# Kernel tuning notes

Hardware: AMD Instinct MI355X
Metric: run time of the kernel (lower is better)

The kernel has to match this reference:

```python
import jax, jax.numpy as jnp
import numpy as np

B, U1, U2 = 2, 3072, 3072
IF = 256      # in_feat_dim
FD = 256      # feat_dim
M = 4         # num_modes
D = IF // M   # attention_mode_dim = 64
STD = 0.02    # base_initializer_range
LN_EPS = 1e-12


def setup_inputs() -> dict:
    key = jax.random.key(0)
    ks = jax.random.split(key, 8)
    inp = {
        'query_feat': jax.random.normal(ks[0], (B, U1, IF), jnp.float32),
        'key_feat':   jax.random.normal(ks[1], (B, U2, IF), jnp.float32),
        # tied QK projection (key weight == query weight after tie_qk)
        'Wq':    jax.random.normal(ks[2], (M * D, IF), jnp.float32) * STD,
        # value projection of ExpandedFeatTrans.first_linear (v_has_bias=True)
        'Wv':    jax.random.normal(ks[3], (M * FD, IF), jnp.float32) * STD,
        'bv':    jnp.zeros((M * FD,), jnp.float32),
        # MMSharedMid shared linear
        'W_mid': jax.random.normal(ks[4], (FD, FD), jnp.float32) * STD,
        'b_mid': jnp.zeros((FD,), jnp.float32),
        # MMSharedOutput shared linear + LayerNorm
        'W_out': jax.random.normal(ks[5], (FD, FD), jnp.float32) * STD,
        'b_out': jnp.zeros((FD,), jnp.float32),
        'ln_g':  jnp.ones((FD,), jnp.float32),
        'ln_b':  jnp.zeros((FD,), jnp.float32),
        # LearnedSoftAggregate feat2score linear (FD -> 1)
        'W_agg': jax.random.normal(ks[6], (1, FD), jnp.float32) * STD,
        'b_agg': jnp.zeros((1,), jnp.float32),
    }
    return inp


def _layer_norm(x, g, b):
    mu = x.mean(-1, keepdims=True)
    var = ((x - mu) ** 2).mean(-1, keepdims=True)
    return (x - mu) * jax.lax.rsqrt(var + LN_EPS) * g + b


def reference(query_feat, key_feat, Wq, Wv, bv, W_mid, b_mid, W_out, b_out,
              ln_g, ln_b, W_agg, b_agg):
    # --- multi-mode cross attention with tied QK ---
    q = (query_feat @ Wq.T).reshape(B, U1, M, D).transpose(0, 2, 1, 3)  # b m u d
    k = (key_feat   @ Wq.T).reshape(B, U2, M, D).transpose(0, 2, 1, 3)  # b m v d
    scores = jnp.einsum('bmud,bmvd->bmuv', q, k) / np.float32(np.sqrt(D))
    probs = jax.nn.softmax(scores, axis=-1)                              # b m u v

    # --- ExpandedFeatTrans: per-mode value projection + fusion ---
    v = (key_feat @ Wv.T + bv).reshape(B, U2, M, FD).transpose(0, 2, 1, 3)  # b m v f
    fused = jnp.einsum('bmuv,bmvf->bmuf', probs, v)                          # b m u f

    # --- MMSharedMid FFN (shared linear + exact gelu; dropout=0) ---
    mid = jax.nn.gelu(fused @ W_mid.T + b_mid, approximate=False)

    # --- MMSharedOutput: shared linear + residual + LayerNorm ---
    outp = _layer_norm(mid @ W_out.T + b_out + fused, ln_g, ln_b)            # b m u f

    # --- LearnedSoftAggregate over modes (group_dim=1) ---
    mode_scores = (outp @ W_agg.T + b_agg)[..., 0]                           # b m u
    agg_probs = jax.nn.softmax(mode_scores, axis=1)
    trans_feat = (outp * agg_probs[..., None]).sum(axis=1)                   # b u f
    return trans_feat
```

## Files before the change

kernel.cpp:

```cpp
#include <hip/hip_runtime.h>
#include <hip/hip_bf16.h>
#include <cstdint>
#include <cstddef>

typedef __attribute__((ext_vector_type(8))) short     bf16x8;
typedef __attribute__((ext_vector_type(4))) float     f32x4;
typedef __attribute__((ext_vector_type(4))) unsigned short u16x4;

using as1_void = __attribute__((address_space(1))) void;
using as3_void = __attribute__((address_space(3))) void;

#define MFMA16(a,b,c) __builtin_amdgcn_mfma_f32_16x16x32_bf16((a),(b),(c),0,0,0)

__device__ __forceinline__ unsigned short f2bf(float f) {
  union { float f; unsigned u; } v; v.f = f;
  unsigned r = v.u + 0x7fffu + ((v.u >> 16) & 1u);
  return (unsigned short)(r >> 16);
}
__device__ __forceinline__ float bf2f(unsigned short h) {
  union { unsigned u; float f; } v; v.u = ((unsigned)h) << 16; return v.f;
}
__device__ __forceinline__ unsigned cvt_pk_bf16(float lo, float hi) {
  unsigned r;
  asm volatile("v_cvt_pk_bf16_f32 %0, %1, %2" : "=v"(r) : "v"(lo), "v"(hi));
  return r;
}
__device__ __forceinline__ float fast_erf(float x) {
  float ax = fabsf(x);
  float t = __builtin_amdgcn_rcpf(fmaf(0.3275911f, ax, 1.0f));
  float p = fmaf(1.061405429f, t, -1.453152027f);
  p = fmaf(p, t, 1.421413741f);
  p = fmaf(p, t, -0.284496736f);
  p = fmaf(p, t, 0.254829592f);
  p = p * t;
  float e = __builtin_amdgcn_exp2f(-ax * ax * 1.44269504f);
  float r = fmaf(-p, e, 1.0f);
  return copysignf(r, x);
}

__device__ __forceinline__ void gload16(const void* g, void* l) {
  __builtin_amdgcn_global_load_lds((const as1_void*)g, (as3_void*)l, 16, 0, 0);
}

constexpr size_t oXq  = 0;
constexpr size_t oXk  = oXq + 1572864ull * 2;
constexpr size_t oWq  = oXk + 1572864ull * 2;
constexpr size_t oWv  = oWq + 65536ull   * 2;
constexpr size_t oWm  = oWv + 262144ull  * 2;
constexpr size_t oWo  = oWm + 65536ull   * 2;
constexpr size_t oQb  = oWo + 65536ull   * 2;
constexpr size_t oKb  = oQb + 1572864ull * 2;
constexpr size_t oVb  = oKb + 1572864ull * 2;
constexpr size_t oPa  = oVb + 6291456ull * 2;
constexpr size_t oMl  = oPa + 12582912ull * 2;

__global__ __launch_bounds__(256) void cvtw_kernel(
    const float* __restrict__ wq, const float* __restrict__ wv,
    const float* __restrict__ wm, const float* __restrict__ wo,
    char* __restrict__ wsb) {
  int i4 = (blockIdx.x * 256 + threadIdx.x) * 4;
  const float* src; size_t dsto; int local;
  if (i4 < 65536)        { src = wq; dsto = oWq; local = i4; }
  else if (i4 < 327680)  { src = wv; dsto = oWv; local = i4 - 65536; }
  else if (i4 < 393216)  { src = wm; dsto = oWm; local = i4 - 327680; }
  else                   { src = wo; dsto = oWo; local = i4 - 393216; }
  f32x4 v = *(const f32x4*)(src + local);
  u16x4 o;
  o.x = f2bf(v.x); o.y = f2bf(v.y); o.z = f2bf(v.z); o.w = f2bf(v.w);
  *(u16x4*)((unsigned short*)(wsb + dsto) + local) = o;
}

__global__ __launch_bounds__(256, 3) void proj_kernel(
    const float* __restrict__ qf32, const float* __restrict__ kf32,
    const float* __restrict__ bv, char* __restrict__ wsb) {
  __shared__ unsigned short sA[48 * 256];

  const int lane = threadIdx.x & 63, wid = threadIdx.x >> 6;
  const int lq = lane & 15, hi = lane >> 4;
  const int ny = blockIdx.x % 6;
  const int r0 = (blockIdx.x / 6) * 48;

  const float* Xf = (ny == 0) ? qf32 : kf32;
  const unsigned short* W;
  if (ny <= 1) W = (const unsigned short*)(wsb + oWq);
  else         W = (const unsigned short*)(wsb + oWv) + (size_t)(ny - 2) * 256 * 256;

  {
    const int t = threadIdx.x;
#pragma unroll
    for (int j = 0; j < 12; ++j) {
      int flat = j * 256 + t;
      int row = flat >> 6;
      int c4 = flat & 63;
      f32x4 v = *(const f32x4*)(Xf + ((size_t)(r0 + row) * 256 + c4 * 4));
      u16x4 o;
      o.x = f2bf(v.x); o.y = f2bf(v.y); o.z = f2bf(v.z); o.w = f2bf(v.w);
      int col = c4 * 4;
      int c8 = col >> 3;
      *(u16x4*)&sA[row * 256 + (((c8 ^ (row & 7)) << 3) + (col & 7))] = o;
    }
  }
  __syncthreads();

  const int n0 = wid * 64;

  f32x4 acc[3][4];
#pragma unroll
  for (int rg = 0; rg < 3; ++rg)
#pragma unroll
    for (int bt = 0; bt < 4; ++bt) acc[rg][bt] = (f32x4){0.f, 0.f, 0.f, 0.f};

#pragma unroll
  for (int ks = 0; ks < 8; ++ks) {
    bf16x8 a[3];
#pragma unroll
    for (int rg = 0; rg < 3; ++rg)
      a[rg] = *(const bf16x8*)&sA[(rg * 16 + lq) * 256 + (((ks * 4 + hi) ^ (lq & 7)) << 3)];
#pragma unroll
    for (int bt = 0; bt < 4; ++bt) {
      int n = n0 + bt * 16 + lq;
      bf16x8 bfr = *(const bf16x8*)(W + (size_t)n * 256 + ks * 32 + hi * 8);
#pragma unroll
      for (int rg = 0; rg < 3; ++rg) acc[rg][bt] = MFMA16(a[rg], bfr, acc[rg][bt]);
    }
  }

  const int b = r0 / 3072, u0 = r0 % 3072;

  if (ny <= 1) {
    unsigned short* outp = (unsigned short*)(wsb + (ny == 0 ? oQb : oKb));
    float scale = (ny == 0) ? 0.125f : 1.0f;
    int m = wid;
#pragma unroll
    for (int bt = 0; bt < 4; ++bt) {
      int d = bt * 16 + lq;
#pragma unroll
      for (int rg = 0; rg < 3; ++rg) {
        int ub = u0 + rg * 16 + hi * 4;
#pragma unroll
        for (int r = 0; r < 4; ++r) {
          outp[((size_t)(b * 4 + m) * 3072 + (ub + r)) * 64 + d] = f2bf(acc[rg][bt][r] * scale);
        }
      }
    }
  } else {
    unsigned short* vbT = (unsigned short*)(wsb + oVb);
    int mchunk = ny - 2;
#pragma unroll
    for (int bt = 0; bt < 4; ++bt) {
      int f = n0 + bt * 16 + lq;
      float bias = bv[mchunk * 256 + f];
#pragma unroll
      for (int rg = 0; rg < 3; ++rg) {
        int ub = u0 + rg * 16 + hi * 4;
        u16x4 pk;
#pragma unroll
        for (int r = 0; r < 4; ++r) pk[r] = f2bf(acc[rg][bt][r] + bias);
        *(u16x4*)(vbT + ((size_t)(b * 4 + mchunk) * 256 + f) * 3072 + ub) = pk;
      }
    }
  }
}

__global__ __launch_bounds__(256, 3) void attn_kernel(char* __restrict__ wsb) {
  __shared__ unsigned short sK[64 * 64];
  __shared__ unsigned short sV[256 * 64];
  __shared__ unsigned short sP[4][16 * 64];
  __shared__ float sCr[4];
  __shared__ float sInv[4][16];

  const int lane = threadIdx.x & 63, wid = threadIdx.x >> 6;
  const int lq = lane & 15, hi = lane >> 4;
  const int lr3 = lane >> 3, lc3 = lane & 7;
  const int fh = wid >> 1, gp = wid & 1;
  const int bm = blockIdx.x & 7;
  const int z = blockIdx.x >> 3;
  const int qt = z >> 1, kvh = z & 1;
  const int q0 = qt * 64;
  const int kvbase = kvh * 1536;
  const int key = lq & 7;

  const unsigned short* qb = (const unsigned short*)(wsb + oQb) + (size_t)bm * 3072 * 64;
  const unsigned short* kb = (const unsigned short*)(wsb + oKb) + (size_t)bm * 3072 * 64;
  const unsigned short* vb = (const unsigned short*)(wsb + oVb) + (size_t)bm * 256 * 3072;

  const unsigned short* qp = qb + (size_t)(q0 + wid * 16 + lq) * 64 + hi * 8;
  const bf16x8 qf0 = *(const bf16x8*)(qp);
  const bf16x8 qf1 = *(const bf16x8*)(qp + 32);

  const unsigned short* pk[2];
  unsigned short* dk[2];
#pragma unroll
  for (int i = 0; i < 2; ++i) {
    int ch = wid * 2 + i;
    int r = ch * 8 + lr3;
    int cs = lc3 ^ (r & 7);
    pk[i] = kb + (size_t)(kvbase + r) * 64 + cs * 8;
    dk[i] = &sK[ch * 512];
  }
  const unsigned short* pv[8];
  unsigned short* dv[8];
#pragma unroll
  for (int i = 0; i < 8; ++i) {
    int ch = i * 4 + wid;
    int f = ch * 8 + lr3;
    int cs = lc3 ^ (f & 7);
    pv[i] = vb + (size_t)f * 3072 + kvbase + cs * 8;
    dv[i] = &sV[ch * 512];
  }

  const int o0 = (hi ^ key) << 4;
  const int o1 = ((hi + 4) ^ key) << 4;
  const char* kB0 = (const char*)sK + lq * 128 + o0;
  const char* kB1 = (const char*)sK + lq * 128 + o1;
  const char* vB0 = (const char*)sV + (size_t)(fh * 128 + lq) * 128 + o0;
  const char* vB1 = (const char*)sV + (size_t)(fh * 128 + lq) * 128 + o1;
  char* myP = (char*)&sP[wid][0] + lq * 128;
  int wofs[4];
#pragma unroll
  for (int t = 0; t < 4; ++t)
    wofs[t] = ((((2 * t + (hi >> 1)) ^ key) << 4) + ((hi & 1) << 3));
  const int g0 = gp * 2, g1 = gp * 2 + 1;
  const char* rP0 = (const char*)&sP[g0][0] + lq * 128;
  const char* rP1 = (const char*)&sP[g1][0] + lq * 128;

  f32x4 acc[2][8];
#pragma unroll
  for (int g = 0; g < 2; ++g)
#pragma unroll
    for (int ft = 0; ft < 8; ++ft) acc[g][ft] = (f32x4){0.f, 0.f, 0.f, 0.f};
  float mrun = -1e30f, lrun = 0.f;

  gload16(pk[0], dk[0]); gload16(pk[1], dk[1]);
  pk[0] += 4096; pk[1] += 4096;
  asm volatile("s_waitcnt vmcnt(0)" ::: "memory");
  __builtin_amdgcn_sched_barrier(0);
  __builtin_amdgcn_s_barrier();

  for (int kt = 0; kt < 24; ++kt) {
#pragma unroll
    for (int i = 0; i < 8; ++i) { gload16(pv[i], dv[i]); pv[i] += 64; }

    bf16x8 kc0[4], kc1[4];
#pragma unroll
    for (int t = 0; t < 4; ++t) {
      kc0[t] = *(const bf16x8*)(kB0 + t * 2048);
      kc1[t] = *(const bf16x8*)(kB1 + t * 2048);
    }
    f32x4 s[4];
#pragma unroll
    for (int t = 0; t < 4; ++t) {
      f32x4 zz = (f32x4){0.f, 0.f, 0.f, 0.f};
      zz = MFMA16(kc0[t], qf0, zz);
      zz = MFMA16(kc1[t], qf1, zz);
      s[t] = zz;
    }

    float p0 = fmaxf(fmaxf(s[0][0], s[0][1]), fmaxf(s[0][2], s[0][3]));
    float p1 = fmaxf(fmaxf(s[1][0], s[1][1]), fmaxf(s[1][2], s[1][3]));
    float p2 = fmaxf(fmaxf(s[2][0], s[2][1]), fmaxf(s[2][2], s[2][3]));
    float p3 = fmaxf(fmaxf(s[3][0], s[3][1]), fmaxf(s[3][2], s[3][3]));
    float pmax = fmaxf(fmaxf(p0, p1), fmaxf(p2, p3));
    pmax = fmaxf(pmax, __shfl_xor(pmax, 16));
    pmax = fmaxf(pmax, __shfl_xor(pmax, 32));

    float cr = 1.0f;
    if (__any(pmax > mrun + 8.0f)) {
      float mnew = fmaxf(mrun, pmax);
      cr = __builtin_amdgcn_exp2f((mrun - mnew) * 1.44269504f);
      lrun *= cr; mrun = mnew;
    }
    if (lane == 0) sCr[wid] = cr;

    const float mk = mrun * 1.44269504f;
    float ps[4][4];
    float psum = 0.f;
#pragma unroll
    for (int t = 0; t < 4; ++t)
#pragma unroll
      for (int r = 0; r < 4; ++r) {
        float p = __builtin_amdgcn_exp2f(s[t][r] * 1.44269504f - mk);
        ps[t][r] = p; psum += p;
      }
    psum += __shfl_xor(psum, 16);
    psum += __shfl_xor(psum, 32);
    lrun += psum;

#pragma unroll
    for (int t = 0; t < 4; ++t) {
      unsigned w0 = cvt_pk_bf16(ps[t][0], ps[t][1]);
      unsigned w1 = cvt_pk_bf16(ps[t][2], ps[t][3]);
      *(uint2*)(myP + wofs[t]) = make_uint2(w0, w1);
    }

    asm volatile("s_waitcnt vmcnt(0) lgkmcnt(0)" ::: "memory");
    __builtin_amdgcn_sched_barrier(0);
    __builtin_amdgcn_s_barrier();

    if (kt < 23) {
      gload16(pk[0], dk[0]); gload16(pk[1], dk[1]);
      pk[0] += 4096; pk[1] += 4096;
    }

    float c0 = sCr[g0], c1 = sCr[g1];
    if (c0 != 1.0f) {
#pragma unroll
      for (int ft = 0; ft < 8; ++ft) {
        acc[0][ft][0] *= c0; acc[0][ft][1] *= c0;
        acc[0][ft][2] *= c0; acc[0][ft][3] *= c0;
      }
    }
    if (c1 != 1.0f) {
#pragma unroll
      for (int ft = 0; ft < 8; ++ft) {
        acc[1][ft][0] *= c1; acc[1][ft][1] *= c1;
        acc[1][ft][2] *= c1; acc[1][ft][3] *= c1;
      }
    }

    bf16x8 pb00 = *(const bf16x8*)(rP0 + o0);
    bf16x8 pb01 = *(const bf16x8*)(rP0 + o1);
    bf16x8 pb10 = *(const bf16x8*)(rP1 + o0);
    bf16x8 pb11 = *(const bf16x8*)(rP1 + o1);

    __builtin_amdgcn_s_setprio(1);
#pragma unroll
    for (int ft = 0; ft < 8; ++ft) {
      bf16x8 vf0 = *(const bf16x8*)(vB0 + ft * 2048);
      bf16x8 vf1 = *(const bf16x8*)(vB1 + ft * 2048);
      acc[0][ft] = MFMA16(vf0, pb00, acc[0][ft]);
      acc[0][ft] = MFMA16(vf1, pb01, acc[0][ft]);
      acc[1][ft] = MFMA16(vf0, pb10, acc[1][ft]);
      acc[1][ft] = MFMA16(vf1, pb11, acc[1][ft]);
    }
    __builtin_amdgcn_s_setprio(0);

    asm volatile("s_waitcnt vmcnt(0) lgkmcnt(0)" ::: "memory");
    __builtin_amdgcn_sched_barrier(0);
    __builtin_amdgcn_s_barrier();
  }

  if (hi == 0) {
    sInv[wid][lq] = 1.0f / lrun;
    float* ml = (float*)(wsb + oMl);
    size_t qi = (size_t)(kvh * 8 + bm) * 3072 + q0 + wid * 16 + lq;
    *(float2*)(ml + qi * 2) = make_float2(mrun, lrun);
  }
  __syncthreads();

  unsigned short* paB = (unsigned short*)(wsb + oPa) + (size_t)(kvh * 8 + bm) * 3072 * 256;
#pragma unroll
  for (int gi = 0; gi < 2; ++gi) {
    int g = gp * 2 + gi;
    float inv = sInv[g][lq];
    unsigned short* orow = paB + (size_t)(q0 + g * 16 + lq) * 256 + fh * 128 + hi * 4;
#pragma unroll
    for (int ft = 0; ft < 8; ++ft) {
      u16x4 pk4;
#pragma unroll
      for (int r = 0; r < 4; ++r) pk4[r] = f2bf(acc[gi][ft][r] * inv);
      *(u16x4*)(orow + ft * 16) = pk4;
    }
  }
}

__global__ __launch_bounds__(256, 3) void ffn_kernel(char* __restrict__ wsb,
                                                     const float* __restrict__ bmid,
                                                     const float* __restrict__ bout,
                                                     const float* __restrict__ lng,
                                                     const float* __restrict__ lnb,
                                                     const float* __restrict__ wagg,
                                                     const float* __restrict__ bagg,
                                                     float* __restrict__ out) {
  __shared__ unsigned short sA[32 * 256];
  __shared__ unsigned short sM[32 * 256];
  __shared__ float redS[4][32], redQ[4][32], redC[4][32];
  __shared__ float sSc[32];
  __shared__ float sW0[32], sW1[32];

  const int lane = threadIdx.x & 63, wid = threadIdx.x >> 6;
  const int lq = lane & 15, hi = lane >> 4;
  const int b = blockIdx.x / 384;
  const int u0 = (blockIdx.x % 384) * 8;

  const unsigned short* Wm = (const unsigned short*)(wsb + oWm);
  const unsigned short* Wo = (const unsigned short*)(wsb + oWo);
  const unsigned short* pa = (const unsigned short*)(wsb + oPa);
  const float* mlb = (const float*)(wsb + oMl);

  if (threadIdx.x < 32) {
    int m = threadIdx.x & 3, du = threadIdx.x >> 2;
    size_t qi = (size_t)(b * 4 + m) * 3072 + u0 + du;
    float2 ml0 = *(const float2*)(mlb + qi * 2);
    float2 ml1 = *(const float2*)(mlb + (qi + 8ull * 3072) * 2);
    float M = fmaxf(ml0.x, ml1.x);
    float e0 = ml0.y * __builtin_amdgcn_exp2f((ml0.x - M) * 1.44269504f);
    float e1 = ml1.y * __builtin_amdgcn_exp2f((ml1.x - M) * 1.44269504f);
    float inv = 1.0f / (e0 + e1);
    sW0[threadIdx.x] = e0 * inv;
    sW1[threadIdx.x] = e1 * inv;
  }
  __syncthreads();

  {
    int t = threadIdx.x;
#pragma unroll
    for (int j = 0; j < 4; ++j) {
      int i = j * 256 + t;
      int row = i >> 5, c = i & 31;
      int m = row & 3, du = row >> 2;
      const unsigned short* p0 = pa + ((size_t)(b * 4 + m) * 3072 + u0 + du) * 256 + c * 8;
      bf16x8 a = *(const bf16x8*)(p0);
      bf16x8 bb = *(const bf16x8*)(p0 + 8ull * 3072 * 256);
      float w0 = sW0[row], w1 = sW1[row];
      u16x4 oA, oB;
#pragma unroll
      for (int e = 0; e < 4; ++e) {
        oA[e] = f2bf(w0 * bf2f((unsigned short)a[e]) + w1 * bf2f((unsigned short)bb[e]));
        oB[e] = f2bf(w0 * bf2f((unsigned short)a[e + 4]) + w1 * bf2f((unsigned short)bb[e + 4]));
      }
      unsigned short* dst = &sA[row * 256 + ((c ^ (row & 7)) << 3)];
      *(u16x4*)(dst) = oA;
      *(u16x4*)(dst + 4) = oB;
    }
  }
  __syncthreads();

  const int n0 = wid * 64;
  const int rowb = hi * 4;

  f32x4 acc1[2][4];
#pragma unroll
  for (int rg = 0; rg < 2; ++rg)
#pragma unroll
    for (int bt = 0; bt < 4; ++bt) acc1[rg][bt] = (f32x4){0.f, 0.f, 0.f, 0.f};
#pragma unroll
  for (int ks = 0; ks < 8; ++ks) {
    bf16x8 a[2];
#pragma unroll
    for (int rg = 0; rg < 2; ++rg)
      a[rg] = *(const bf16x8*)&sA[(rg * 16 + lq) * 256 + (((ks * 4 + hi) ^ (lq & 7)) << 3)];
#pragma unroll
    for (int bt = 0; bt < 4; ++bt) {
      int n = n0 + bt * 16 + lq;
      bf16x8 bfr = *(const bf16x8*)(Wm + (size_t)n * 256 + ks * 32 + hi * 8);
#pragma unroll
      for (int rg = 0; rg < 2; ++rg) acc1[rg][bt] = MFMA16(a[rg], bfr, acc1[rg][bt]);
    }
  }
#pragma unroll
  for (int bt = 0; bt < 4; ++bt) {
    int n = n0 + bt * 16 + lq;
    float bb = bmid[n];
#pragma unroll
    for (int rg = 0; rg < 2; ++rg)
#pragma unroll
      for (int r = 0; r < 4; ++r) {
        float x = acc1[rg][bt][r] + bb;
        float g = 0.5f * x * (1.0f + fast_erf(x * 0.7071067811865475f));
        int row = rg * 16 + rowb + r;
        sM[row * 256 + (((n >> 3) ^ (row & 7)) << 3) + (n & 7)] = f2bf(g);
      }
  }
  __syncthreads();

  f32x4 acc2[2][4];
#pragma unroll
  for (int rg = 0; rg < 2; ++rg)
#pragma unroll
    for (int bt = 0; bt < 4; ++bt) acc2[rg][bt] = (f32x4){0.f, 0.f, 0.f, 0.f};
#pragma unroll
  for (int ks = 0; ks < 8; ++ks) {
    bf16x8 a[2];
#pragma unroll
    for (int rg = 0; rg < 2; ++rg)
      a[rg] = *(const bf16x8*)&sM[(rg * 16 + lq) * 256 + (((ks * 4 + hi) ^ (lq & 7)) << 3)];
#pragma unroll
    for (int bt = 0; bt < 4; ++bt) {
      int n = n0 + bt * 16 + lq;
      bf16x8 bfr = *(const bf16x8*)(Wo + (size_t)n * 256 + ks * 32 + hi * 8);
#pragma unroll
      for (int rg = 0; rg < 2; ++rg) acc2[rg][bt] = MFMA16(a[rg], bfr, acc2[rg][bt]);
    }
  }

  float sS[2][4], sQ[2][4];
#pragma unroll
  for (int rg = 0; rg < 2; ++rg)
#pragma unroll
    for (int r = 0; r < 4; ++r) { sS[rg][r] = 0.f; sQ[rg][r] = 0.f; }
#pragma unroll
  for (int bt = 0; bt < 4; ++bt) {
    int n = n0 + bt * 16 + lq;
    float bo = bout[n];
#pragma unroll
    for (int rg = 0; rg < 2; ++rg)
#pragma unroll
      for (int r = 0; r < 4; ++r) {
        int row = rg * 16 + rowb + r;
        float res = bf2f(sA[row * 256 + (((n >> 3) ^ (row & 7)) << 3) + (n & 7)]);
        float x = acc2[rg][bt][r] + bo + res;
        acc2[rg][bt][r] = x;
        sS[rg][r] += x;
        sQ[rg][r] += x * x;
      }
  }
#pragma unroll
  for (int rg = 0; rg < 2; ++rg)
#pragma unroll
    for (int r = 0; r < 4; ++r) {
#pragma unroll
      for (int off = 1; off < 16; off <<= 1) {
        sS[rg][r] += __shfl_xor(sS[rg][r], off);
        sQ[rg][r] += __shfl_xor(sQ[rg][r], off);
      }
    }
  if (lq == 0) {
#pragma unroll
    for (int rg = 0; rg < 2; ++rg)
#pragma unroll
      for (int r = 0; r < 4; ++r) {
        int row = rg * 16 + rowb + r;
        redS[wid][row] = sS[rg][r]; redQ[wid][row] = sQ[rg][r];
      }
  }
  __syncthreads();

  float scp[2][4];
#pragma unroll
  for (int rg = 0; rg < 2; ++rg)
#pragma unroll
    for (int r = 0; r < 4; ++r) {
      int row = rg * 16 + rowb + r;
      float ts = redS[0][row] + redS[1][row] + redS[2][row] + redS[3][row];
      float tq = redQ[0][row] + redQ[1][row] + redQ[2][row] + redQ[3][row];
      float mean = ts * (1.0f / 256.0f);
      float var = tq * (1.0f / 256.0f) - mean * mean;
      float rs = rsqrtf(var + 1e-12f);
      float sc = 0.f;
#pragma unroll
      for (int bt = 0; bt < 4; ++bt) {
        int n = n0 + bt * 16 + lq;
        float o = (acc2[rg][bt][r] - mean) * rs * lng[n] + lnb[n];
        acc2[rg][bt][r] = o;
        sc += o * wagg[n];
      }
      scp[rg][r] = sc;
    }
#pragma unroll
  for (int rg = 0; rg < 2; ++rg)
#pragma unroll
    for (int r = 0; r < 4; ++r) {
#pragma unroll
      for (int off = 1; off < 16; off <<= 1) scp[rg][r] += __shfl_xor(scp[rg][r], off);
    }
  if (lq == 0) {
#pragma unroll
    for (int rg = 0; rg < 2; ++rg)
#pragma unroll
      for (int r = 0; r < 4; ++r) redC[wid][rg * 16 + rowb + r] = scp[rg][r];
  }
  __syncthreads();

  if (threadIdx.x < 32) {
    int t = threadIdx.x;
    sSc[t] = redC[0][t] + redC[1][t] + redC[2][t] + redC[3][t] + bagg[0];
  }
  __syncthreads();

  float wm[2][4];
#pragma unroll
  for (int rg = 0; rg < 2; ++rg) {
    int du = rg * 4 + hi;
    float s0 = sSc[du * 4 + 0], s1 = sSc[du * 4 + 1];
    float s2 = sSc[du * 4 + 2], s3 = sSc[du * 4 + 3];
    float mx = fmaxf(fmaxf(s0, s1), fmaxf(s2, s3));
    float e0 = __builtin_amdgcn_exp2f((s0 - mx) * 1.44269504f);
    float e1 = __builtin_amdgcn_exp2f((s1 - mx) * 1.44269504f);
    float e2 = __builtin_amdgcn_exp2f((s2 - mx) * 1.44269504f);
    float e3 = __builtin_amdgcn_exp2f((s3 - mx) * 1.44269504f);
    float inv = 1.0f / (e0 + e1 + e2 + e3);
    wm[rg][0] = e0 * inv; wm[rg][1] = e1 * inv;
    wm[rg][2] = e2 * inv; wm[rg][3] = e3 * inv;
  }
#pragma unroll
  for (int bt = 0; bt < 4; ++bt) {
    int n = n0 + bt * 16 + lq;
#pragma unroll
    for (int rg = 0; rg < 2; ++rg) {
      int du = rg * 4 + hi;
      float val = wm[rg][0] * acc2[rg][bt][0] + wm[rg][1] * acc2[rg][bt][1]
                + wm[rg][2] * acc2[rg][bt][2] + wm[rg][3] * acc2[rg][bt][3];
      out[((size_t)(b * 3072 + u0 + du)) * 256 + n] = val;
    }
  }
}

extern "C" void kernel_launch(void* const* d_in, const int* in_sizes, int n_in,
                              void* d_out, int out_size, void* d_ws, size_t ws_size,
                              hipStream_t stream) {
  const float* q  = (const float*)d_in[0];
  const float* k  = (const float*)d_in[1];
  const float* wq = (const float*)d_in[2];
  const float* wv = (const float*)d_in[3];
  const float* bv = (const float*)d_in[4];
  const float* wm = (const float*)d_in[5];
  const float* bm = (const float*)d_in[6];
  const float* wo = (const float*)d_in[7];
  const float* bo = (const float*)d_in[8];
  const float* lg = (const float*)d_in[9];
  const float* lb = (const float*)d_in[10];
  const float* wa = (const float*)d_in[11];
  const float* ba = (const float*)d_in[12];
  char* wsb = (char*)d_ws;

  cvtw_kernel<<<448, 256, 0, stream>>>(wq, wv, wm, wo, wsb);
  proj_kernel<<<768, 256, 0, stream>>>(q, k, bv, wsb);
  attn_kernel<<<768, 256, 0, stream>>>(wsb);
  ffn_kernel<<<768, 256, 0, stream>>>(wsb, bm, bo, lg, lb, wa, ba, (float*)d_out);
}
```

Before: 128.8 us.

## Load V tiles directly from global into registers instead of staging through LDS

V operand fragments are now read straight from global memory into registers per wave, removing the sV shared-memory buffer and its async global-to-LDS copies. The first half of V is loaded before the score computation and the second half after the barrier, and the first barrier's wait no longer drains vmcnt. This frees LDS and LDS bandwidth, but V data shared by the two wave pairs with the same fh is now fetched twice from global/L2, and register pressure rises with the 16 bf16x8 fragments held per iteration.

```diff
diff --git a/kernel.cpp b/kernel.cpp
--- a/kernel.cpp
+++ b/kernel.cpp
@@ -164,7 +164,6 @@
 
 __global__ __launch_bounds__(256, 3) void attn_kernel(char* __restrict__ wsb) {
   __shared__ unsigned short sK[64 * 64];
-  __shared__ unsigned short sV[256 * 64];
   __shared__ unsigned short sP[4][16 * 64];
   __shared__ float sCr[4];
   __shared__ float sInv[4][16];
@@ -198,23 +197,14 @@
     pk[i] = kb + (size_t)(kvbase + r) * 64 + cs * 8;
     dk[i] = &sK[ch * 512];
   }
-  const unsigned short* pv[8];
-  unsigned short* dv[8];
-#pragma unroll
-  for (int i = 0; i < 8; ++i) {
-    int ch = i * 4 + wid;
-    int f = ch * 8 + lr3;
-    int cs = lc3 ^ (f & 7);
-    pv[i] = vb + (size_t)f * 3072 + kvbase + cs * 8;
-    dv[i] = &sV[ch * 512];
-  }
+
+  const unsigned short* vq0 = vb + (size_t)(fh * 128 + lq) * 3072 + kvbase + hi * 8;
+  const unsigned short* vq1 = vq0 + 32;
 
   const int o0 = (hi ^ key) << 4;
   const int o1 = ((hi + 4) ^ key) << 4;
   const char* kB0 = (const char*)sK + lq * 128 + o0;
   const char* kB1 = (const char*)sK + lq * 128 + o1;
-  const char* vB0 = (const char*)sV + (size_t)(fh * 128 + lq) * 128 + o0;
-  const char* vB1 = (const char*)sV + (size_t)(fh * 128 + lq) * 128 + o1;
   char* myP = (char*)&sP[wid][0] + lq * 128;
   int wofs[4];
 #pragma unroll
@@ -238,8 +228,12 @@
   __builtin_amdgcn_s_barrier();
 
   for (int kt = 0; kt < 24; ++kt) {
-#pragma unroll
-    for (int i = 0; i < 8; ++i) { gload16(pv[i], dv[i]); pv[i] += 64; }
+    bf16x8 vf0[8];
+    {
+      const unsigned short* p = vq0;
+#pragma unroll
+      for (int ft = 0; ft < 8; ++ft) { vf0[ft] = *(const bf16x8*)p; p += 16 * 3072; }
+    }
 
     bf16x8 kc0[4], kc1[4];
 #pragma unroll
@@ -293,9 +287,16 @@
       *(uint2*)(myP + wofs[t]) = make_uint2(w0, w1);
     }
 
-    asm volatile("s_waitcnt vmcnt(0) lgkmcnt(0)" ::: "memory");
+    asm volatile("s_waitcnt lgkmcnt(0)" ::: "memory");
     __builtin_amdgcn_sched_barrier(0);
     __builtin_amdgcn_s_barrier();
+
+    bf16x8 vf1[8];
+    {
+      const unsigned short* p = vq1;
+#pragma unroll
+      for (int ft = 0; ft < 8; ++ft) { vf1[ft] = *(const bf16x8*)p; p += 16 * 3072; }
+    }
 
     if (kt < 23) {
       gload16(pk[0], dk[0]); gload16(pk[1], dk[1]);
@@ -326,18 +327,21 @@
     __builtin_amdgcn_s_setprio(1);
 #pragma unroll
     for (int ft = 0; ft < 8; ++ft) {
-      bf16x8 vf0 = *(const bf16x8*)(vB0 + ft * 2048);
-      bf16x8 vf1 = *(const bf16x8*)(vB1 + ft * 2048);
-      acc[0][ft] = MFMA16(vf0, pb00, acc[0][ft]);
-      acc[0][ft] = MFMA16(vf1, pb01, acc[0][ft]);
-      acc[1][ft] = MFMA16(vf0, pb10, acc[1][ft]);
-      acc[1][ft] = MFMA16(vf1, pb11, acc[1][ft]);
+      acc[0][ft] = MFMA16(vf0[ft], pb00, acc[0][ft]);
+      acc[1][ft] = MFMA16(vf0[ft], pb10, acc[1][ft]);
+    }
+#pragma unroll
+    for (int ft = 0; ft < 8; ++ft) {
+      acc[0][ft] = MFMA16(vf1[ft], pb01, acc[0][ft]);
+      acc[1][ft] = MFMA16(vf1[ft], pb11, acc[1][ft]);
     }
     __builtin_amdgcn_s_setprio(0);
 
     asm volatile("s_waitcnt vmcnt(0) lgkmcnt(0)" ::: "memory");
     __builtin_amdgcn_sched_barrier(0);
     __builtin_amdgcn_s_barrier();
+
+    vq0 += 64; vq1 += 64;
   }
 
   if (hi == 0) {
```

New measurement: 234.7 us. +82.2%, slower.
